# Kernel tuning notes

Hardware: AMD Instinct MI355X
Metric: run time of the kernel (lower is better)

Reference implementation:

```python
import jax, jax.numpy as jnp
import numpy as np

N = 10000      # nodes
E0 = 100000    # edges (no self loops); self loops appended -> E = E0 + N
IN = 512       # input feature dim
HID = 256      # out_channels per head
OUT = 10       # classes
H1, H2 = 4, 1  # heads conv1 / conv2
K = 5          # mixture-of-Gaussians prior components ('mixGau-5')
ON = 2 * HID   # out_neurons per head (mean | raw-std)
D1, D2 = H1 * HID, H2 * HID  # latent dims per conv
LOG2PI = float(np.log(2.0 * np.pi))


def _norm_logprob(z, mu, sigma):
    return -0.5 * jnp.square((z - mu) / sigma) - jnp.log(sigma) - 0.5 * LOG2PI


def _seg_softmax(logits, seg, n):
    # numerically stable softmax over segments defined by seg (target node ids)
    m = jax.ops.segment_max(logits, seg, num_segments=n)
    e = jnp.exp(logits - m[seg])
    s = jax.ops.segment_sum(e, seg, num_segments=n)
    return e / (s[seg] + 1e-16)


def _gib_conv(x, W, att, pi, mu, logsig, eps, gumbel, src, dst, heads):
    n = x.shape[0]
    xh = (x @ W).reshape(n, heads, ON)                       # [n,H,ON]
    # GAT attention: score(e) = leaky_relu(<x_i,att_l> + <x_j,att_r>)
    s_i = jnp.einsum('nhd,hd->nh', xh, att[:, :ON])
    s_j = jnp.einsum('nhd,hd->nh', xh, att[:, ON:])
    alpha = jax.nn.leaky_relu(s_i[dst] + s_j[src], 0.2)      # [E,H]
    alpha = _seg_softmax(alpha, dst, n)
    # structure KL vs uniform prior 1/deg
    deg = jax.ops.segment_sum(jnp.ones_like(alpha[:, 0]), dst, num_segments=n)
    prior = (1.0 / deg)[dst][:, None]
    kl = (alpha * (jnp.log(alpha + 1e-12) - jnp.log(prior + 1e-12))).sum() / alpha.size
    # categorical structural sampling: gumbel-softmax per segment
    alpha_s = _seg_softmax(jnp.log(alpha + 1e-16) + gumbel, dst, n)
    out = jax.ops.segment_sum(xh[src] * alpha_s[:, :, None], dst, num_segments=n)  # [n,H,ON]
    # per-head diag reparameterization: ON = (mean:HID | raw std:HID)
    mean = out[..., :HID].reshape(n, heads * HID)
    std = jax.nn.softplus(out[..., HID:]).reshape(n, heads * HID) + 1e-10
    Z = mean[None] + std[None] * eps                         # [S,n,D]
    log_q = _norm_logprob(Z, mean[None], std[None]).sum(-1)  # [S,n]
    # mixture-of-Gaussians feature prior, per-dimension mixture
    logpi = jax.nn.log_softmax(pi)
    comp = _norm_logprob(Z[..., None], mu, jnp.exp(logsig)) + logpi  # [S,n,D,K]
    prior_lp = jax.nn.logsumexp(comp, axis=-1).sum(-1)       # [S,n]
    ixz = (log_q - prior_lp).mean()
    return Z.mean(0), kl, ixz


def setup_inputs() -> dict:
    key = jax.random.key(0)
    ks = jax.random.split(key, 20)
    x = jax.random.normal(ks[0], (N, IN), jnp.float32)
    # edge list guaranteed free of self-loops (remove_self_loops is then a no-op)
    s = jax.random.randint(ks[1], (E0,), 0, N)
    off = jax.random.randint(ks[2], (E0,), 1, N)
    edge_index = jnp.stack([s, (s + off) % N]).astype(jnp.int32)
    E = E0 + N

    def xav(k, fi, fo):
        a = np.sqrt(6.0 / (fi + fo)).astype(np.float32)
        return jax.random.uniform(k, (fi, fo), jnp.float32, -a, a)

    def gumbel(k, shape):
        u = jax.random.uniform(k, shape, jnp.float32, 1e-6, 1.0 - 1e-6)
        return -jnp.log(-jnp.log(u))

    return {
        'x': x, 'edge_index': edge_index,
        'W1': xav(ks[3], IN, H1 * ON),
        'att1': xav(ks[4], H1, 2 * ON),
        'pi1': jnp.zeros((K,), jnp.float32),
        'mu1': jax.random.normal(ks[5], (D1, K), jnp.float32) * 0.1,
        'logsig1': jnp.zeros((D1, K), jnp.float32),
        'eps1': jax.random.normal(ks[6], (1, N, D1), jnp.float32),
        'g1': gumbel(ks[7], (E, H1)),
        'W2': xav(ks[8], D1, H2 * ON),
        'att2': xav(ks[9], H2, 2 * ON),
        'pi2': jnp.zeros((K,), jnp.float32),
        'mu2': jax.random.normal(ks[10], (D2, K), jnp.float32) * 0.1,
        'logsig2': jnp.zeros((D2, K), jnp.float32),
        'eps2': jax.random.normal(ks[11], (1, N, D2), jnp.float32),
        'g2': gumbel(ks[12], (E, H2)),
        'Wfc': xav(ks[13], D2, OUT),
        'bfc': jnp.zeros((OUT,), jnp.float32),
    }


def reference(x, edge_index, W1, att1, pi1, mu1, logsig1, eps1, g1,
              W2, att2, pi2, mu2, logsig2, eps2, g2, Wfc, bfc):
    n = x.shape[0]
    loop = jnp.arange(n, dtype=edge_index.dtype)
    src = jnp.concatenate([edge_index[0], loop])
    dst = jnp.concatenate([edge_index[1], loop])
    h, kl1, ixz1 = _gib_conv(x, W1, att1, pi1, mu1, logsig1, eps1, g1, src, dst, H1)
    h = jax.nn.elu(h)
    h, kl2, ixz2 = _gib_conv(h, W2, att2, pi2, mu2, logsig2, eps2, g2, src, dst, H2)
    h = jax.nn.elu(h)
    logits = h @ Wfc + bfc
    return logits, kl1 + kl2, ixz1 + ixz2
```

## Files before the change

kernel.cpp:

```cpp
#include <hip/hip_runtime.h>
#include <math.h>

constexpr int NN   = 10000;
constexpr int E0C  = 100000;
constexpr int EC   = E0C + NN;
constexpr int INC  = 512;
constexpr int HIDC = 256;
constexpr int OUTC = 10;
constexpr int H1C  = 4;
constexpr int H2C  = 1;
constexpr int ONC  = 2 * HIDC;
constexpr int D1C  = H1C * HIDC;
constexpr int D2C  = H2C * HIDC;
constexpr int KC   = 5;
constexpr float LOG2PI_F = 1.8378770664093453f;

using u16 = unsigned short;
typedef __attribute__((ext_vector_type(8))) short bf16x8;
typedef __attribute__((ext_vector_type(4))) float f32x4;

__device__ __forceinline__ unsigned fkey(float f) {
    unsigned b = __float_as_uint(f);
    return (b & 0x80000000u) ? ~b : (b | 0x80000000u);
}
__device__ __forceinline__ float funkey(unsigned k) {
    unsigned b = (k & 0x80000000u) ? (k & 0x7fffffffu) : ~k;
    return __uint_as_float(b);
}
__device__ __forceinline__ unsigned f2bf(float f) {
    unsigned u = __float_as_uint(f);
    return (u + 0x7fffu + ((u >> 16) & 1u)) >> 16;
}
__device__ __forceinline__ float bflo(unsigned u) { return __uint_as_float(u << 16); }
__device__ __forceinline__ float bfhi(unsigned u) { return __uint_as_float(u & 0xffff0000u); }
__device__ __forceinline__ float bf1(u16 v) { return __uint_as_float(((unsigned)v) << 16); }
__device__ __forceinline__ void edge_sd(int e, const int* __restrict__ ei, int& src, int& dst) {
    if (e < E0C) { src = ei[e]; dst = ei[E0C + e]; }
    else         { src = e - E0C; dst = src; }
}

__global__ void zero_u32(unsigned* __restrict__ p, int n) {
    int i = blockIdx.x * blockDim.x + threadIdx.x;
    if (i < n) p[i] = 0u;
}

__global__ void cast_bf16(const float* __restrict__ in, u16* __restrict__ o, int n4) {
    int i = blockIdx.x * blockDim.x + threadIdx.x;
    if (i >= n4) return;
    float4 v = ((const float4*)in)[i];
    uint2 r;
    r.x = f2bf(v.x) | (f2bf(v.y) << 16);
    r.y = f2bf(v.z) | (f2bf(v.w) << 16);
    ((uint2*)o)[i] = r;
}

__global__ __launch_bounds__(256) void transpose_cast_bf16(const float* __restrict__ W,
                                                           u16* __restrict__ WT,
                                                           int K, int N) {
    __shared__ float tile[32][33];
    int n0 = blockIdx.x * 32, k0 = blockIdx.y * 32;
    int tx = threadIdx.x, ty = threadIdx.y;
    for (int r = ty; r < 32; r += 8) tile[r][tx] = W[(size_t)(k0 + r) * N + n0 + tx];
    __syncthreads();
    for (int r = ty; r < 32; r += 8) WT[(size_t)(n0 + r) * K + k0 + tx] = (u16)f2bf(tile[tx][r]);
}

__global__ void count_deg(const int* __restrict__ ei, int* __restrict__ deg) {
    int e = blockIdx.x * blockDim.x + threadIdx.x;
    if (e >= EC) return;
    int dst = (e < E0C) ? ei[E0C + e] : (e - E0C);
    atomicAdd(&deg[dst], 1);
}

__global__ __launch_bounds__(1024) void scan_kernel(const int* __restrict__ deg,
                                                    int* __restrict__ offs,
                                                    float* __restrict__ deg_f) {
    __shared__ int part[1024];
    const int CH = (NN + 1023) / 1024;
    int tid = threadIdx.x;
    int base = tid * CH;
    int s = 0;
    for (int i = 0; i < CH; i++) { int idx = base + i; if (idx < NN) s += deg[idx]; }
    part[tid] = s;
    __syncthreads();
    for (int o = 1; o < 1024; o <<= 1) {
        int v = (tid >= o) ? part[tid - o] : 0;
        __syncthreads();
        part[tid] += v;
        __syncthreads();
    }
    int run = (tid == 0) ? 0 : part[tid - 1];
    for (int i = 0; i < CH; i++) {
        int idx = base + i;
        if (idx < NN) {
            offs[idx] = run;
            run += deg[idx];
            deg_f[idx] = (float)deg[idx];
        }
    }
    if (tid == 1023) offs[NN] = run;
}

__global__ void csr_fill(const int* __restrict__ ei, int* __restrict__ cursor,
                         const int* __restrict__ offs, int* __restrict__ csr_src,
                         int* __restrict__ pos_of_e) {
    int e = blockIdx.x * blockDim.x + threadIdx.x;
    if (e >= EC) return;
    int src, dst;
    edge_sd(e, ei, src, dst);
    int pos = offs[dst] + atomicAdd(&cursor[dst], 1);
    csr_src[pos] = src;
    pos_of_e[e] = pos;
}

template <int BM, int BN, int BK, bool BF16OUT>
__global__ __launch_bounds__(256) void mfma_gemm(const u16* __restrict__ A,
                                                 const u16* __restrict__ BT,
                                                 void* __restrict__ Cv,
                                                 int M, int N, int K) {
    constexpr int PK = BK + 16;
    __shared__ __align__(16) u16 As[BM][PK];
    __shared__ __align__(16) u16 Bs[BN][PK];
    const int tid = threadIdx.x;
    const int lane = tid & 63;
    const int wave = tid >> 6;
    const int wm = (wave & 1) * 64;
    const int wn = (wave >> 1) * 64;
    const int row0 = blockIdx.y * BM;
    const int col0 = blockIdx.x * BN;

    f32x4 acc[4][4] = {};
    const int srow = tid >> 1;
    const int shalf = (tid & 1) * 16;
    const int fr = lane & 15;
    const int fq = (lane >> 4) * 8;

    for (int k0 = 0; k0 < K; k0 += BK) {
        uint4 va0 = {0, 0, 0, 0}, va1 = {0, 0, 0, 0};
        int ga = row0 + srow;
        if (ga < M) {
            const uint4* p = (const uint4*)(A + (size_t)ga * K + k0 + shalf);
            va0 = p[0]; va1 = p[1];
        }
        const uint4* pb = (const uint4*)(BT + (size_t)(col0 + srow) * K + k0 + shalf);
        uint4 vb0 = pb[0], vb1 = pb[1];
        __syncthreads();
        *(uint4*)&As[srow][shalf]     = va0;
        *(uint4*)&As[srow][shalf + 8] = va1;
        *(uint4*)&Bs[srow][shalf]     = vb0;
        *(uint4*)&Bs[srow][shalf + 8] = vb1;
        __syncthreads();
        bf16x8 af[4], bfr[4];
#pragma unroll
        for (int i = 0; i < 4; i++) {
            af[i]  = *(const bf16x8*)&As[wm + i * 16 + fr][fq];
            bfr[i] = *(const bf16x8*)&Bs[wn + i * 16 + fr][fq];
        }
#pragma unroll
        for (int mi = 0; mi < 4; mi++)
#pragma unroll
            for (int ni = 0; ni < 4; ni++)
                acc[mi][ni] = __builtin_amdgcn_mfma_f32_16x16x32_bf16(af[mi], bfr[ni], acc[mi][ni], 0, 0, 0);
    }
    const int cc = lane & 15;
    const int cr = (lane >> 4) * 4;
#pragma unroll
    for (int mi = 0; mi < 4; mi++) {
#pragma unroll
        for (int r = 0; r < 4; r++) {
            int grow = row0 + wm + mi * 16 + cr + r;
            if (grow < M) {
#pragma unroll
                for (int ni = 0; ni < 4; ni++) {
                    int gcol = col0 + wn + ni * 16 + cc;
                    if (BF16OUT)
                        ((u16*)Cv)[(size_t)grow * N + gcol] = (u16)f2bf(acc[mi][ni][r]);
                    else
                        ((float*)Cv)[(size_t)grow * N + gcol] = acc[mi][ni][r];
                }
            }
        }
    }
}

template <int H>
__global__ __launch_bounds__(256) void scores_bf16(const u16* __restrict__ xh,
                                                   const float* __restrict__ att,
                                                   float* __restrict__ s_i,
                                                   float* __restrict__ s_j) {
    int gw = (blockIdx.x * 256 + threadIdx.x) >> 6;
    int lane = threadIdx.x & 63;
    if (gw >= NN * H) return;
    int n = gw / H, h = gw - n * H;
    const u16* xr = xh + ((size_t)n * H + h) * ONC;
    uint4 v = ((const uint4*)xr)[lane];
    float xv[8] = { bflo(v.x), bfhi(v.x), bflo(v.y), bfhi(v.y),
                    bflo(v.z), bfhi(v.z), bflo(v.w), bfhi(v.w) };
    const float* base = att + (size_t)h * 2 * ONC;
    const float4* aL = (const float4*)(base + lane * 8);
    const float4* aR = (const float4*)(base + ONC + lane * 8);
    float4 l0 = aL[0], l1 = aL[1], r0 = aR[0], r1 = aR[1];
    float ai = xv[0] * l0.x + xv[1] * l0.y + xv[2] * l0.z + xv[3] * l0.w
             + xv[4] * l1.x + xv[5] * l1.y + xv[6] * l1.z + xv[7] * l1.w;
    float aj = xv[0] * r0.x + xv[1] * r0.y + xv[2] * r0.z + xv[3] * r0.w
             + xv[4] * r1.x + xv[5] * r1.y + xv[6] * r1.z + xv[7] * r1.w;
#pragma unroll
    for (int o = 32; o > 0; o >>= 1) {
        ai += __shfl_down(ai, o, 64);
        aj += __shfl_down(aj, o, 64);
    }
    if (lane == 0) { s_i[gw] = ai; s_j[gw] = aj; }
}

template <int H>
__global__ void edge_pass1(const int* __restrict__ ei, const float* __restrict__ s_i,
                           const float* __restrict__ s_j, float* __restrict__ A,
                           unsigned* __restrict__ m1) {
    int idx = blockIdx.x * blockDim.x + threadIdx.x;
    if (idx >= EC * H) return;
    int e = idx / H, h = idx - e * H;
    int src, dst; edge_sd(e, ei, src, dst);
    float a = s_i[dst * H + h] + s_j[src * H + h];
    a = (a > 0.f) ? a : 0.2f * a;
    A[idx] = a;
    atomicMax(&m1[dst * H + h], fkey(a));
}

template <int H>
__global__ void edge_pass2(const int* __restrict__ ei, float* __restrict__ A,
                           const unsigned* __restrict__ m1, float* __restrict__ ss1) {
    int idx = blockIdx.x * blockDim.x + threadIdx.x;
    if (idx >= EC * H) return;
    int e = idx / H, h = idx - e * H;
    int src, dst; edge_sd(e, ei, src, dst);
    float ex = __expf(A[idx] - funkey(m1[dst * H + h]));
    A[idx] = ex;
    atomicAdd(&ss1[dst * H + h], ex);
}

template <int H>
__global__ __launch_bounds__(256) void edge_pass3(const int* __restrict__ ei,
                                                  const float* __restrict__ A,
                                                  const float* __restrict__ ss1,
                                                  const float* __restrict__ deg_f,
                                                  const float* __restrict__ g,
                                                  float* __restrict__ B,
                                                  unsigned* __restrict__ m2,
                                                  float* __restrict__ kl_acc,
                                                  float scale) {
    int idx = blockIdx.x * blockDim.x + threadIdx.x;
    float t = 0.f;
    if (idx < EC * H) {
        int e = idx / H, h = idx - e * H;
        int src, dst; edge_sd(e, ei, src, dst);
        float alpha = A[idx] / (ss1[dst * H + h] + 1e-16f);
        float prior = 1.0f / deg_f[dst];
        t = alpha * (__logf(alpha + 1e-12f) - __logf(prior + 1e-12f));
        float l2 = __logf(alpha + 1e-16f) + g[idx];
        B[idx] = l2;
        atomicMax(&m2[dst * H + h], fkey(l2));
    }
#pragma unroll
    for (int o = 32; o > 0; o >>= 1) t += __shfl_down(t, o, 64);
    __shared__ float red[4];
    int lane = threadIdx.x & 63, wid = threadIdx.x >> 6;
    if (lane == 0) red[wid] = t;
    __syncthreads();
    if (threadIdx.x == 0) {
        atomicAdd(kl_acc, (red[0] + red[1] + red[2] + red[3]) * scale);
    }
}

template <int H>
__global__ void edge_pass4(const int* __restrict__ ei, float* __restrict__ B,
                           const unsigned* __restrict__ m2, float* __restrict__ ss2) {
    int idx = blockIdx.x * blockDim.x + threadIdx.x;
    if (idx >= EC * H) return;
    int e = idx / H, h = idx - e * H;
    int src, dst; edge_sd(e, ei, src, dst);
    float ex = __expf(B[idx] - funkey(m2[dst * H + h]));
    B[idx] = ex;
    atomicAdd(&ss2[dst * H + h], ex);
}

template <int H>
__global__ void edge_pass5(const int* __restrict__ ei, const float* __restrict__ B,
                           const float* __restrict__ ss2, const int* __restrict__ pos_of_e,
                           float* __restrict__ Bp) {
    int idx = blockIdx.x * blockDim.x + threadIdx.x;
    if (idx >= EC * H) return;
    int e = idx / H, h = idx - e * H;
    int src, dst; edge_sd(e, ei, src, dst);
    Bp[(size_t)pos_of_e[e] * H + h] = B[idx] / (ss2[dst * H + h] + 1e-16f);
}

template <int H>
__global__ __launch_bounds__(256) void gather_bf16(const u16* __restrict__ xh,
                                                   const float* __restrict__ alpha_csr,
                                                   const int* __restrict__ offs,
                                                   const int* __restrict__ csr_src,
                                                   u16* __restrict__ out) {
    constexpr int CPE = H * ONC / 256;
    constexpr int CHK = 128;
    int n = blockIdx.x;
    int tid = threadIdx.x;
    int beg = offs[n], end = offs[n + 1];
    __shared__ int s_src[CHK];
    __shared__ __align__(16) float s_w[CHK][H];
    float acc[CPE];
#pragma unroll
    for (int j = 0; j < CPE; j++) acc[j] = 0.f;
    const int c0 = tid * CPE;
    const int head = c0 / ONC;
    for (int c = beg; c < end; c += CHK) {
        int cnt = min(CHK, end - c);
        __syncthreads();
        for (int i = tid; i < cnt; i += 256) {
            s_src[i] = csr_src[c + i];
            if (H == 4) {
                float4 w = ((const float4*)alpha_csr)[c + i];
                *(float4*)s_w[i] = w;
            } else {
                s_w[i][0] = alpha_csr[c + i];
            }
        }
        __syncthreads();
        for (int i = 0; i < cnt; i++) {
            const u16* xr = xh + (size_t)s_src[i] * (H * ONC) + c0;
            float w = s_w[i][head];
            if (CPE == 8) {
                uint4 v = *(const uint4*)xr;
                acc[0] = fmaf(w, bflo(v.x), acc[0]);
                acc[1] = fmaf(w, bfhi(v.x), acc[1]);
                acc[2] = fmaf(w, bflo(v.y), acc[2]);
                acc[3] = fmaf(w, bfhi(v.y), acc[3]);
                acc[4] = fmaf(w, bflo(v.z), acc[4]);
                acc[5] = fmaf(w, bfhi(v.z), acc[5]);
                acc[6] = fmaf(w, bflo(v.w), acc[6]);
                acc[7] = fmaf(w, bfhi(v.w), acc[7]);
            } else {
                unsigned v = *(const unsigned*)xr;
                acc[0] = fmaf(w, bflo(v), acc[0]);
                acc[1] = fmaf(w, bfhi(v), acc[1]);
            }
        }
    }
    u16* orow = out + (size_t)n * (H * ONC) + c0;
    if (CPE == 8) {
        uint4 r;
        r.x = f2bf(acc[0]) | (f2bf(acc[1]) << 16);
        r.y = f2bf(acc[2]) | (f2bf(acc[3]) << 16);
        r.z = f2bf(acc[4]) | (f2bf(acc[5]) << 16);
        r.w = f2bf(acc[6]) | (f2bf(acc[7]) << 16);
        *(uint4*)orow = r;
    } else {
        *(unsigned*)orow = f2bf(acc[0]) | (f2bf(acc[1]) << 16);
    }
}

__global__ void mix_table(const float* __restrict__ pi, const float* __restrict__ mu,
                          const float* __restrict__ logsig, float* __restrict__ tab, int DK) {
    int i = blockIdx.x * blockDim.x + threadIdx.x;
    if (i >= DK) return;
    int k = i % KC;
    float p[KC]; float mx = -3.4e38f;
#pragma unroll
    for (int j = 0; j < KC; j++) { p[j] = pi[j]; mx = fmaxf(mx, p[j]); }
    float s = 0.f;
#pragma unroll
    for (int j = 0; j < KC; j++) s += expf(p[j] - mx);
    float lpi = p[k] - (mx + logf(s));
    float ls = logsig[i];
    float inv = expf(-ls);
    float inv2 = inv * inv;
    float m = mu[i];
    tab[i]          = -0.5f * inv2;
    tab[DK + i]     = inv2 * m;
    tab[2 * DK + i] = -0.5f * inv2 * m * m - ls - 0.5f * LOG2PI_F + lpi;
}

template <int H, int NT, bool BF16OUT>
__global__ __launch_bounds__(256) void zixz3_kernel(const u16* __restrict__ in_agg,
                                                    const float* __restrict__ eps,
                                                    const float* __restrict__ tab,
                                                    void* __restrict__ hout_,
                                                    float* __restrict__ ixz_acc) {
    constexpr int D = H * HIDC;
    constexpr int DK = D * KC;
    const int tid = threadIdx.x;
    const int h = blockIdx.y;
    const int d = h * HIDC + tid;
    float ca[KC], cb[KC], cc[KC];
#pragma unroll
    for (int k = 0; k < KC; k++) {
        ca[k] = tab[d * KC + k];
        cb[k] = tab[DK + d * KC + k];
        cc[k] = tab[2 * DK + d * KC + k];
    }
    const int n0 = blockIdx.x * NT;
    float local = 0.f;
#pragma unroll 1
    for (int nn = 0; nn < NT; nn++) {
        int n = n0 + nn;
        const u16* orow = in_agg + ((size_t)n * H + h) * ONC;
        float mean = bf1(orow[tid]);
        float raw  = bf1(orow[HIDC + tid]);
        float sp = fmaxf(raw, 0.f) + __logf(1.f + __expf(-fabsf(raw)));
        float stdv = sp + 1e-10f;
        float ep = eps[(size_t)n * D + d];
        float Z = fmaf(stdv, ep, mean);
        float hv = (Z > 0.f) ? Z : (__expf(Z) - 1.f);
        if (BF16OUT) ((u16*)hout_)[(size_t)n * D + d] = (u16)f2bf(hv);
        else         ((float*)hout_)[(size_t)n * D + d] = hv;
        float logq = fmaf(-0.5f, ep * ep, -__logf(stdv)) - 0.5f * LOG2PI_F;
        float comp[KC]; float mx = -3.4e38f;
#pragma unroll
        for (int k = 0; k < KC; k++) {
            float cv = fmaf(fmaf(ca[k], Z, cb[k]), Z, cc[k]);
            comp[k] = cv;
            mx = fmaxf(mx, cv);
        }
        float se = 0.f;
#pragma unroll
        for (int k = 0; k < KC; k++) se += __expf(comp[k] - mx);
        local += logq - (mx + __logf(se));
    }
#pragma unroll
    for (int o = 32; o > 0; o >>= 1) local += __shfl_down(local, o, 64);
    __shared__ float red[4];
    int lane = tid & 63, wid = tid >> 6;
    if (lane == 0) red[wid] = local;
    __syncthreads();
    if (tid == 0) {
        atomicAdd(ixz_acc, (red[0] + red[1] + red[2] + red[3]) * (1.0f / NN));
    }
}

__global__ void fc_kernel(const float* __restrict__ h, const float* __restrict__ W,
                          const float* __restrict__ b, float* __restrict__ out) {
    int idx = blockIdx.x * blockDim.x + threadIdx.x;
    if (idx >= NN * OUTC) return;
    int n = idx / OUTC, o = idx - n * OUTC;
    const float* hr = h + (size_t)n * D2C;
    float acc = b[o];
#pragma unroll 8
    for (int c = 0; c < D2C; c++) acc += hr[c] * W[c * OUTC + o];
    out[idx] = acc;
}

extern "C" void kernel_launch(void* const* d_in, const int* in_sizes, int n_in,
                              void* d_out, int out_size, void* d_ws, size_t ws_size,
                              hipStream_t stream) {
    (void)in_sizes; (void)n_in; (void)out_size; (void)ws_size;
    const float* x       = (const float*)d_in[0];
    const int*   ei      = (const int*)d_in[1];
    const float* W1      = (const float*)d_in[2];
    const float* att1    = (const float*)d_in[3];
    const float* pi1     = (const float*)d_in[4];
    const float* mu1     = (const float*)d_in[5];
    const float* logsig1 = (const float*)d_in[6];
    const float* eps1    = (const float*)d_in[7];
    const float* g1      = (const float*)d_in[8];
    const float* W2      = (const float*)d_in[9];
    const float* att2    = (const float*)d_in[10];
    const float* pi2     = (const float*)d_in[11];
    const float* mu2     = (const float*)d_in[12];
    const float* logsig2 = (const float*)d_in[13];
    const float* eps2    = (const float*)d_in[14];
    const float* g2      = (const float*)d_in[15];
    const float* Wfc     = (const float*)d_in[16];
    const float* bfc     = (const float*)d_in[17];
    float* out = (float*)d_out;

    char* ws = (char*)d_ws;
    const size_t szAB = (size_t)NN * 2048 * sizeof(float);
    char* regA = ws;
    char* regB = ws + szAB;
    size_t cur = 2 * szAB;
    auto alloc = [&](size_t bytes) -> char* {
        char* p = ws + cur;
        cur += (bytes + 255) & ~(size_t)255;
        return p;
    };
    float*    alphaA  = (float*)alloc((size_t)EC * H1C * sizeof(float));
    float*    alphaB  = (float*)alloc((size_t)EC * H1C * sizeof(float));
    float*    s_i     = (float*)alloc((size_t)NN * H1C * sizeof(float));
    float*    s_j     = (float*)alloc((size_t)NN * H1C * sizeof(float));
    unsigned* stats   = (unsigned*)alloc((size_t)4 * NN * H1C * sizeof(unsigned));
    unsigned* m1  = stats;
    float*    ss1 = (float*)(stats + (size_t)NN * H1C);
    unsigned* m2  = stats + (size_t)2 * NN * H1C;
    float*    ss2 = (float*)(stats + (size_t)3 * NN * H1C);
    int*   deg_i    = (int*)alloc(NN * sizeof(int));
    float* deg_f    = (float*)alloc(NN * sizeof(float));
    int*   offs     = (int*)alloc((NN + 1) * sizeof(int));
    int*   cursor   = (int*)alloc(NN * sizeof(int));
    int*   csr_src  = (int*)alloc(EC * sizeof(int));
    int*   pos_of_e = (int*)alloc(EC * sizeof(int));
    u16*   xb1     = (u16*)alloc((size_t)NN * INC * sizeof(u16));
    u16*   w1t     = (u16*)alloc((size_t)2048 * 512 * sizeof(u16));
    u16*   w2t     = (u16*)alloc((size_t)512 * 1024 * sizeof(u16));
    float* tab1    = (float*)alloc((size_t)3 * D1C * KC * sizeof(float));
    float* tab2    = (float*)alloc((size_t)3 * D2C * KC * sizeof(float));

    u16*   xh1b = (u16*)regA;
    u16*   out1 = (u16*)regB;
    u16*   h1b  = (u16*)regA;
    u16*   xh2b = (u16*)regB;
    u16*   out2 = (u16*)regA;
    float* h2   = (float*)(regB + (size_t)NN * 512 * sizeof(u16));
    float* kl_acc  = out + (size_t)NN * OUTC;
    float* ixz_acc = kl_acc + 1;

    const int ZB = 256;
    zero_u32<<<(NN + ZB - 1) / ZB, ZB, 0, stream>>>((unsigned*)deg_i, NN);
    zero_u32<<<(NN + ZB - 1) / ZB, ZB, 0, stream>>>((unsigned*)cursor, NN);
    zero_u32<<<(4 * NN * H1C + ZB - 1) / ZB, ZB, 0, stream>>>(stats, 4 * NN * H1C);
    zero_u32<<<1, ZB, 0, stream>>>((unsigned*)kl_acc, 2);

    count_deg<<<(EC + ZB - 1) / ZB, ZB, 0, stream>>>(ei, deg_i);
    scan_kernel<<<1, 1024, 0, stream>>>(deg_i, offs, deg_f);
    csr_fill<<<(EC + ZB - 1) / ZB, ZB, 0, stream>>>(ei, cursor, offs, csr_src, pos_of_e);

    cast_bf16<<<(NN * INC / 4 + ZB - 1) / ZB, ZB, 0, stream>>>(x, xb1, NN * INC / 4);
    transpose_cast_bf16<<<dim3(2048 / 32, 512 / 32), dim3(32, 8), 0, stream>>>(W1, w1t, 512, 2048);
    transpose_cast_bf16<<<dim3(512 / 32, 1024 / 32), dim3(32, 8), 0, stream>>>(W2, w2t, 1024, 512);
    mix_table<<<(D1C * KC + ZB - 1) / ZB, ZB, 0, stream>>>(pi1, mu1, logsig1, tab1, D1C * KC);
    mix_table<<<(D2C * KC + ZB - 1) / ZB, ZB, 0, stream>>>(pi2, mu2, logsig2, tab2, D2C * KC);

    const int EB1 = (EC * H1C + ZB - 1) / ZB;
    const int EB2 = (EC * H2C + ZB - 1) / ZB;
    const int MG = (NN + 127) / 128;

    mfma_gemm<128, 128, 32, true><<<dim3(2048 / 128, MG), 256, 0, stream>>>(xb1, w1t, xh1b, NN, 2048, 512);
    scores_bf16<H1C><<<(NN * H1C + 3) / 4, 256, 0, stream>>>(xh1b, att1, s_i, s_j);
    edge_pass1<H1C><<<EB1, ZB, 0, stream>>>(ei, s_i, s_j, alphaA, m1);
    edge_pass2<H1C><<<EB1, ZB, 0, stream>>>(ei, alphaA, m1, ss1);
    edge_pass3<H1C><<<EB1, ZB, 0, stream>>>(ei, alphaA, ss1, deg_f, g1, alphaA, m2, kl_acc,
                                            1.0f / (float)(EC * H1C));
    edge_pass4<H1C><<<EB1, ZB, 0, stream>>>(ei, alphaA, m2, ss2);
    edge_pass5<H1C><<<EB1, ZB, 0, stream>>>(ei, alphaA, ss2, pos_of_e, alphaB);
    gather_bf16<H1C><<<NN, 256, 0, stream>>>(xh1b, alphaB, offs, csr_src, out1);
    zixz3_kernel<H1C, 25, true><<<dim3(NN / 25, H1C), 256, 0, stream>>>(out1, eps1, tab1, (void*)h1b, ixz_acc);

    zero_u32<<<(4 * NN * H1C + ZB - 1) / ZB, ZB, 0, stream>>>(stats, 4 * NN * H1C);
    mfma_gemm<128, 128, 32, true><<<dim3(512 / 128, MG), 256, 0, stream>>>(h1b, w2t, xh2b, NN, 512, 1024);
    scores_bf16<H2C><<<(NN * H2C + 3) / 4, 256, 0, stream>>>(xh2b, att2, s_i, s_j);
    edge_pass1<H2C><<<EB2, ZB, 0, stream>>>(ei, s_i, s_j, alphaA, m1);
    edge_pass2<H2C><<<EB2, ZB, 0, stream>>>(ei, alphaA, m1, ss1);
    edge_pass3<H2C><<<EB2, ZB, 0, stream>>>(ei, alphaA, ss1, deg_f, g2, alphaA, m2, kl_acc,
                                            1.0f / (float)(EC * H2C));
    edge_pass4<H2C><<<EB2, ZB, 0, stream>>>(ei, alphaA, m2, ss2);
    edge_pass5<H2C><<<EB2, ZB, 0, stream>>>(ei, alphaA, ss2, pos_of_e, alphaB);
    gather_bf16<H2C><<<NN, 256, 0, stream>>>(xh2b, alphaB, offs, csr_src, out2);
    zixz3_kernel<H2C, 10, false><<<dim3(NN / 10, H2C), 256, 0, stream>>>(out2, eps2, tab2, (void*)h2, ixz_acc);

    fc_kernel<<<(NN * OUTC + ZB - 1) / ZB, ZB, 0, stream>>>(h2, Wfc, bfc, out);
}
```

Baseline: 521.5 us.

## Fuse edge softmax passes into per-node CSR wave kernel and panelize gather

Replaces the five per-edge attention passes, which used global atomicMax/atomicAdd on per-node stats, with a single kernel that walks each target node's CSR segment in one wave. It computes both segment softmaxes and the KL term with wave reductions and writes alpha directly in CSR order. The KL is rewritten algebraically using log-sum-exp, which drops the epsilon terms. The gather is also split into column panels with one wave per node, giving more parallel blocks and smaller per-thread loads. This removes atomics, stat zeroing and intermediate edge arrays, but the gumbel reads become indirect, lanes sit idle on low-degree nodes, and each panel block re-reads the same CSR indices.

```diff
diff --git a/kernel.cpp b/kernel.cpp
--- a/kernel.cpp
+++ b/kernel.cpp
@@ -19,14 +19,6 @@
 typedef __attribute__((ext_vector_type(8))) short bf16x8;
 typedef __attribute__((ext_vector_type(4))) float f32x4;
 
-__device__ __forceinline__ unsigned fkey(float f) {
-    unsigned b = __float_as_uint(f);
-    return (b & 0x80000000u) ? ~b : (b | 0x80000000u);
-}
-__device__ __forceinline__ float funkey(unsigned k) {
-    unsigned b = (k & 0x80000000u) ? (k & 0x7fffffffu) : ~k;
-    return __uint_as_float(b);
-}
 __device__ __forceinline__ unsigned f2bf(float f) {
     unsigned u = __float_as_uint(f);
     return (u + 0x7fffu + ((u >> 16) & 1u)) >> 16;
@@ -37,6 +29,16 @@
 __device__ __forceinline__ void edge_sd(int e, const int* __restrict__ ei, int& src, int& dst) {
     if (e < E0C) { src = ei[e]; dst = ei[E0C + e]; }
     else         { src = e - E0C; dst = src; }
+}
+__device__ __forceinline__ float wmax(float x) {
+#pragma unroll
+    for (int o = 32; o > 0; o >>= 1) x = fmaxf(x, __shfl_xor(x, o, 64));
+    return x;
+}
+__device__ __forceinline__ float wsum(float x) {
+#pragma unroll
+    for (int o = 32; o > 0; o >>= 1) x += __shfl_xor(x, o, 64);
+    return x;
 }
 
 __global__ void zero_u32(unsigned* __restrict__ p, int n) {
@@ -73,8 +75,7 @@
 }
 
 __global__ __launch_bounds__(1024) void scan_kernel(const int* __restrict__ deg,
-                                                    int* __restrict__ offs,
-                                                    float* __restrict__ deg_f) {
+                                                    int* __restrict__ offs) {
     __shared__ int part[1024];
     const int CH = (NN + 1023) / 1024;
     int tid = threadIdx.x;
@@ -95,7 +96,6 @@
         if (idx < NN) {
             offs[idx] = run;
             run += deg[idx];
-            deg_f[idx] = (float)deg[idx];
         }
     }
     if (tid == 1023) offs[NN] = run;
@@ -103,14 +103,14 @@
 
 __global__ void csr_fill(const int* __restrict__ ei, int* __restrict__ cursor,
                          const int* __restrict__ offs, int* __restrict__ csr_src,
-                         int* __restrict__ pos_of_e) {
+                         int* __restrict__ csr_eid) {
     int e = blockIdx.x * blockDim.x + threadIdx.x;
     if (e >= EC) return;
     int src, dst;
     edge_sd(e, ei, src, dst);
     int pos = offs[dst] + atomicAdd(&cursor[dst], 1);
     csr_src[pos] = src;
-    pos_of_e[e] = pos;
+    csr_eid[pos] = e;
 }
 
 template <int BM, int BN, int BK, bool BF16OUT>
@@ -212,147 +212,137 @@
     if (lane == 0) { s_i[gw] = ai; s_j[gw] = aj; }
 }
 
-template <int H>
-__global__ void edge_pass1(const int* __restrict__ ei, const float* __restrict__ s_i,
-                           const float* __restrict__ s_j, float* __restrict__ A,
-                           unsigned* __restrict__ m1) {
-    int idx = blockIdx.x * blockDim.x + threadIdx.x;
-    if (idx >= EC * H) return;
-    int e = idx / H, h = idx - e * H;
-    int src, dst; edge_sd(e, ei, src, dst);
-    float a = s_i[dst * H + h] + s_j[src * H + h];
-    a = (a > 0.f) ? a : 0.2f * a;
-    A[idx] = a;
-    atomicMax(&m1[dst * H + h], fkey(a));
-}
-
-template <int H>
-__global__ void edge_pass2(const int* __restrict__ ei, float* __restrict__ A,
-                           const unsigned* __restrict__ m1, float* __restrict__ ss1) {
-    int idx = blockIdx.x * blockDim.x + threadIdx.x;
-    if (idx >= EC * H) return;
-    int e = idx / H, h = idx - e * H;
-    int src, dst; edge_sd(e, ei, src, dst);
-    float ex = __expf(A[idx] - funkey(m1[dst * H + h]));
-    A[idx] = ex;
-    atomicAdd(&ss1[dst * H + h], ex);
-}
-
-template <int H>
-__global__ __launch_bounds__(256) void edge_pass3(const int* __restrict__ ei,
-                                                  const float* __restrict__ A,
-                                                  const float* __restrict__ ss1,
-                                                  const float* __restrict__ deg_f,
+template <int H, int PW>
+__global__ __launch_bounds__(256) void attn_fused(const int* __restrict__ offs,
+                                                  const int* __restrict__ csr_src,
+                                                  const int* __restrict__ csr_eid,
+                                                  const float* __restrict__ s_i,
+                                                  const float* __restrict__ s_j,
                                                   const float* __restrict__ g,
-                                                  float* __restrict__ B,
-                                                  unsigned* __restrict__ m2,
+                                                  float* __restrict__ alpha_csr,
                                                   float* __restrict__ kl_acc,
                                                   float scale) {
-    int idx = blockIdx.x * blockDim.x + threadIdx.x;
-    float t = 0.f;
-    if (idx < EC * H) {
-        int e = idx / H, h = idx - e * H;
-        int src, dst; edge_sd(e, ei, src, dst);
-        float alpha = A[idx] / (ss1[dst * H + h] + 1e-16f);
-        float prior = 1.0f / deg_f[dst];
-        t = alpha * (__logf(alpha + 1e-12f) - __logf(prior + 1e-12f));
-        float l2 = __logf(alpha + 1e-16f) + g[idx];
-        B[idx] = l2;
-        atomicMax(&m2[dst * H + h], fkey(l2));
-    }
-#pragma unroll
-    for (int o = 32; o > 0; o >>= 1) t += __shfl_down(t, o, 64);
+    const int tid = threadIdx.x;
+    const int wave = tid >> 6, lane = tid & 63;
+    const int pair0 = (blockIdx.x * 4 + wave) * PW;
+    float kl = 0.f;
+#pragma unroll 1
+    for (int t = 0; t < PW; t++) {
+        int pr = pair0 + t;
+        if (pr >= NN * H) break;
+        int n = pr / H, h = pr - (pr / H) * H;
+        int beg = offs[n], end = offs[n + 1];
+        int deg = end - beg;
+        float si = s_i[n * H + h];
+        float ldeg = __logf((float)deg);
+        if (deg <= 64) {
+            int pos = beg + lane;
+            bool v = lane < deg;
+            int src = v ? csr_src[pos] : 0;
+            int eid = v ? csr_eid[pos] : 0;
+            float a = si + s_j[src * H + h];
+            a = (a > 0.f) ? a : 0.2f * a;
+            if (!v) a = -3.4e38f;
+            float m1 = wmax(a);
+            float am = v ? (a - m1) : 0.f;
+            float e1 = v ? __expf(am) : 0.f;
+            float ss1 = wsum(e1);
+            float sd  = wsum(e1 * am);
+            float lss1 = __logf(ss1);
+            kl += sd / ss1 - lss1 + ldeg;
+            float l2 = v ? (am - lss1 + g[eid * H + h]) : -3.4e38f;
+            float m2 = wmax(l2);
+            float e2 = v ? __expf(l2 - m2) : 0.f;
+            float ss2 = wsum(e2);
+            if (v) alpha_csr[(size_t)pos * H + h] = e2 / ss2;
+        } else {
+            float m1 = -3.4e38f;
+            for (int p = beg + lane; p < end; p += 64) {
+                float a = si + s_j[csr_src[p] * H + h];
+                a = (a > 0.f) ? a : 0.2f * a;
+                m1 = fmaxf(m1, a);
+            }
+            m1 = wmax(m1);
+            float ss1 = 0.f, sd = 0.f;
+            for (int p = beg + lane; p < end; p += 64) {
+                float a = si + s_j[csr_src[p] * H + h];
+                a = (a > 0.f) ? a : 0.2f * a;
+                float e1 = __expf(a - m1);
+                ss1 += e1; sd += e1 * (a - m1);
+            }
+            ss1 = wsum(ss1); sd = wsum(sd);
+            float lss1 = __logf(ss1);
+            kl += sd / ss1 - lss1 + ldeg;
+            float m2 = -3.4e38f;
+            for (int p = beg + lane; p < end; p += 64) {
+                float a = si + s_j[csr_src[p] * H + h];
+                a = (a > 0.f) ? a : 0.2f * a;
+                m2 = fmaxf(m2, a - m1 - lss1 + g[csr_eid[p] * H + h]);
+            }
+            m2 = wmax(m2);
+            float ss2 = 0.f;
+            for (int p = beg + lane; p < end; p += 64) {
+                float a = si + s_j[csr_src[p] * H + h];
+                a = (a > 0.f) ? a : 0.2f * a;
+                ss2 += __expf(a - m1 - lss1 + g[csr_eid[p] * H + h] - m2);
+            }
+            ss2 = wsum(ss2);
+            for (int p = beg + lane; p < end; p += 64) {
+                float a = si + s_j[csr_src[p] * H + h];
+                a = (a > 0.f) ? a : 0.2f * a;
+                alpha_csr[(size_t)p * H + h] =
+                    __expf(a - m1 - lss1 + g[csr_eid[p] * H + h] - m2) / ss2;
+            }
+        }
+    }
     __shared__ float red[4];
-    int lane = threadIdx.x & 63, wid = threadIdx.x >> 6;
-    if (lane == 0) red[wid] = t;
+    if (lane == 0) red[wave] = kl;
     __syncthreads();
-    if (threadIdx.x == 0) {
+    if (tid == 0)
         atomicAdd(kl_acc, (red[0] + red[1] + red[2] + red[3]) * scale);
-    }
-}
-
-template <int H>
-__global__ void edge_pass4(const int* __restrict__ ei, float* __restrict__ B,
-                           const unsigned* __restrict__ m2, float* __restrict__ ss2) {
-    int idx = blockIdx.x * blockDim.x + threadIdx.x;
-    if (idx >= EC * H) return;
-    int e = idx / H, h = idx - e * H;
-    int src, dst; edge_sd(e, ei, src, dst);
-    float ex = __expf(B[idx] - funkey(m2[dst * H + h]));
-    B[idx] = ex;
-    atomicAdd(&ss2[dst * H + h], ex);
-}
-
-template <int H>
-__global__ void edge_pass5(const int* __restrict__ ei, const float* __restrict__ B,
-                           const float* __restrict__ ss2, const int* __restrict__ pos_of_e,
-                           float* __restrict__ Bp) {
-    int idx = blockIdx.x * blockDim.x + threadIdx.x;
-    if (idx >= EC * H) return;
-    int e = idx / H, h = idx - e * H;
-    int src, dst; edge_sd(e, ei, src, dst);
-    Bp[(size_t)pos_of_e[e] * H + h] = B[idx] / (ss2[dst * H + h] + 1e-16f);
-}
-
-template <int H>
-__global__ __launch_bounds__(256) void gather_bf16(const u16* __restrict__ xh,
-                                                   const float* __restrict__ alpha_csr,
-                                                   const int* __restrict__ offs,
-                                                   const int* __restrict__ csr_src,
-                                                   u16* __restrict__ out) {
-    constexpr int CPE = H * ONC / 256;
-    constexpr int CHK = 128;
-    int n = blockIdx.x;
-    int tid = threadIdx.x;
-    int beg = offs[n], end = offs[n + 1];
-    __shared__ int s_src[CHK];
-    __shared__ __align__(16) float s_w[CHK][H];
-    float acc[CPE];
-#pragma unroll
-    for (int j = 0; j < CPE; j++) acc[j] = 0.f;
-    const int c0 = tid * CPE;
-    const int head = c0 / ONC;
-    for (int c = beg; c < end; c += CHK) {
-        int cnt = min(CHK, end - c);
-        __syncthreads();
-        for (int i = tid; i < cnt; i += 256) {
-            s_src[i] = csr_src[c + i];
-            if (H == 4) {
-                float4 w = ((const float4*)alpha_csr)[c + i];
-                *(float4*)s_w[i] = w;
-            } else {
-                s_w[i][0] = alpha_csr[c + i];
-            }
-        }
-        __syncthreads();
-        for (int i = 0; i < cnt; i++) {
-            const u16* xr = xh + (size_t)s_src[i] * (H * ONC) + c0;
-            float w = s_w[i][head];
-            if (CPE == 8) {
-                uint4 v = *(const uint4*)xr;
-                acc[0] = fmaf(w, bflo(v.x), acc[0]);
-                acc[1] = fmaf(w, bfhi(v.x), acc[1]);
-                acc[2] = fmaf(w, bflo(v.y), acc[2]);
-                acc[3] = fmaf(w, bfhi(v.y), acc[3]);
-                acc[4] = fmaf(w, bflo(v.z), acc[4]);
-                acc[5] = fmaf(w, bfhi(v.z), acc[5]);
-                acc[6] = fmaf(w, bflo(v.w), acc[6]);
-                acc[7] = fmaf(w, bfhi(v.w), acc[7]);
-            } else {
-                unsigned v = *(const unsigned*)xr;
-                acc[0] = fmaf(w, bflo(v), acc[0]);
-                acc[1] = fmaf(w, bfhi(v), acc[1]);
-            }
-        }
-    }
-    u16* orow = out + (size_t)n * (H * ONC) + c0;
-    if (CPE == 8) {
-        uint4 r;
+}
+
+template <int H, int NP>
+__global__ __launch_bounds__(256) void gather_panel(const u16* __restrict__ xh,
+                                                    const float* __restrict__ alpha_csr,
+                                                    const int* __restrict__ offs,
+                                                    const int* __restrict__ csr_src,
+                                                    u16* __restrict__ out) {
+    constexpr int ROW = H * ONC;
+    constexpr int CPP = ROW / NP;
+    constexpr int CL  = CPP / 64;
+    const int bx = blockIdx.x;
+    const int panel = bx % NP;
+    const int n = (bx / NP) * 4 + (threadIdx.x >> 6);
+    const int lane = threadIdx.x & 63;
+    const int head = (panel * CPP) / ONC;
+    const int c0 = panel * CPP + lane * CL;
+    const int beg = offs[n], end = offs[n + 1];
+    float acc[CL];
+#pragma unroll
+    for (int j = 0; j < CL; j++) acc[j] = 0.f;
+    for (int p = beg; p < end; ++p) {
+        int src = csr_src[p];
+        float w = alpha_csr[(size_t)p * H + head];
+        const u16* xr = xh + (size_t)src * ROW + c0;
+        if (CL == 4) {
+            uint2 v = *(const uint2*)xr;
+            acc[0] = fmaf(w, bflo(v.x), acc[0]);
+            acc[1] = fmaf(w, bfhi(v.x), acc[1]);
+            acc[2] = fmaf(w, bflo(v.y), acc[2]);
+            acc[3] = fmaf(w, bfhi(v.y), acc[3]);
+        } else {
+            unsigned v = *(const unsigned*)xr;
+            acc[0] = fmaf(w, bflo(v), acc[0]);
+            acc[1] = fmaf(w, bfhi(v), acc[1]);
+        }
+    }
+    u16* orow = out + (size_t)n * ROW + c0;
+    if (CL == 4) {
+        uint2 r;
         r.x = f2bf(acc[0]) | (f2bf(acc[1]) << 16);
         r.y = f2bf(acc[2]) | (f2bf(acc[3]) << 16);
-        r.z = f2bf(acc[4]) | (f2bf(acc[5]) << 16);
-        r.w = f2bf(acc[6]) | (f2bf(acc[7]) << 16);
-        *(uint4*)orow = r;
+        *(uint2*)orow = r;
     } else {
         *(unsigned*)orow = f2bf(acc[0]) | (f2bf(acc[1]) << 16);
     }
@@ -482,21 +472,14 @@
         cur += (bytes + 255) & ~(size_t)255;
         return p;
     };
-    float*    alphaA  = (float*)alloc((size_t)EC * H1C * sizeof(float));
-    float*    alphaB  = (float*)alloc((size_t)EC * H1C * sizeof(float));
-    float*    s_i     = (float*)alloc((size_t)NN * H1C * sizeof(float));
-    float*    s_j     = (float*)alloc((size_t)NN * H1C * sizeof(float));
-    unsigned* stats   = (unsigned*)alloc((size_t)4 * NN * H1C * sizeof(unsigned));
-    unsigned* m1  = stats;
-    float*    ss1 = (float*)(stats + (size_t)NN * H1C);
-    unsigned* m2  = stats + (size_t)2 * NN * H1C;
-    float*    ss2 = (float*)(stats + (size_t)3 * NN * H1C);
+    float* alphaB   = (float*)alloc((size_t)EC * H1C * sizeof(float));
+    float* s_i      = (float*)alloc((size_t)NN * H1C * sizeof(float));
+    float* s_j      = (float*)alloc((size_t)NN * H1C * sizeof(float));
     int*   deg_i    = (int*)alloc(NN * sizeof(int));
-    float* deg_f    = (float*)alloc(NN * sizeof(float));
     int*   offs     = (int*)alloc((NN + 1) * sizeof(int));
     int*   cursor   = (int*)alloc(NN * sizeof(int));
     int*   csr_src  = (int*)alloc(EC * sizeof(int));
-    int*   pos_of_e = (int*)alloc(EC * sizeof(int));
+    int*   csr_eid  = (int*)alloc(EC * sizeof(int));
     u16*   xb1     = (u16*)alloc((size_t)NN * INC * sizeof(u16));
     u16*   w1t     = (u16*)alloc((size_t)2048 * 512 * sizeof(u16));
     u16*   w2t     = (u16*)alloc((size_t)512 * 1024 * sizeof(u16));
@@ -515,12 +498,11 @@
     const int ZB = 256;
     zero_u32<<<(NN + ZB - 1) / ZB, ZB, 0, stream>>>((unsigned*)deg_i, NN);
     zero_u32<<<(NN + ZB - 1) / ZB, ZB, 0, stream>>>((unsigned*)cursor, NN);
-    zero_u32<<<(4 * NN * H1C + ZB - 1) / ZB, ZB, 0, stream>>>(stats, 4 * NN * H1C);
     zero_u32<<<1, ZB, 0, stream>>>((unsigned*)kl_acc, 2);
 
     count_deg<<<(EC + ZB - 1) / ZB, ZB, 0, stream>>>(ei, deg_i);
-    scan_kernel<<<1, 1024, 0, stream>>>(deg_i, offs, deg_f);
-    csr_fill<<<(EC + ZB - 1) / ZB, ZB, 0, stream>>>(ei, cursor, offs, csr_src, pos_of_e);
+    scan_kernel<<<1, 1024, 0, stream>>>(deg_i, offs);
+    csr_fill<<<(EC + ZB - 1) / ZB, ZB, 0, stream>>>(ei, cursor, offs, csr_src, csr_eid);
 
     cast_bf16<<<(NN * INC / 4 + ZB - 1) / ZB, ZB, 0, stream>>>(x, xb1, NN * INC / 4);
     transpose_cast_bf16<<<dim3(2048 / 32, 512 / 32), dim3(32, 8), 0, stream>>>(W1, w1t, 512, 2048);
@@ -528,31 +510,22 @@
     mix_table<<<(D1C * KC + ZB - 1) / ZB, ZB, 0, stream>>>(pi1, mu1, logsig1, tab1, D1C * KC);
     mix_table<<<(D2C * KC + ZB - 1) / ZB, ZB, 0, stream>>>(pi2, mu2, logsig2, tab2, D2C * KC);
 
-    const int EB1 = (EC * H1C + ZB - 1) / ZB;
-    const int EB2 = (EC * H2C + ZB - 1) / ZB;
     const int MG = (NN + 127) / 128;
 
     mfma_gemm<128, 128, 32, true><<<dim3(2048 / 128, MG), 256, 0, stream>>>(xb1, w1t, xh1b, NN, 2048, 512);
     scores_bf16<H1C><<<(NN * H1C + 3) / 4, 256, 0, stream>>>(xh1b, att1, s_i, s_j);
-    edge_pass1<H1C><<<EB1, ZB, 0, stream>>>(ei, s_i, s_j, alphaA, m1);
-    edge_pass2<H1C><<<EB1, ZB, 0, stream>>>(ei, alphaA, m1, ss1);
-    edge_pass3<H1C><<<EB1, ZB, 0, stream>>>(ei, alphaA, ss1, deg_f, g1, alphaA, m2, kl_acc,
-                                            1.0f / (float)(EC * H1C));
-    edge_pass4<H1C><<<EB1, ZB, 0, stream>>>(ei, alphaA, m2, ss2);
-    edge_pass5<H1C><<<EB1, ZB, 0, stream>>>(ei, alphaA, ss2, pos_of_e, alphaB);
-    gather_bf16<H1C><<<NN, 256, 0, stream>>>(xh1b, alphaB, offs, csr_src, out1);
+    attn_fused<H1C, 8><<<(NN * H1C + 31) / 32, 256, 0, stream>>>(offs, csr_src, csr_eid,
+                                                                 s_i, s_j, g1, alphaB, kl_acc,
+                                                                 1.0f / (float)(EC * H1C));
+    gather_panel<H1C, 8><<<8 * (NN / 4), 256, 0, stream>>>(xh1b, alphaB, offs, csr_src, out1);
     zixz3_kernel<H1C, 25, true><<<dim3(NN / 25, H1C), 256, 0, stream>>>(out1, eps1, tab1, (void*)h1b, ixz_acc);
 
-    zero_u32<<<(4 * NN * H1C + ZB - 1) / ZB, ZB, 0, stream>>>(stats, 4 * NN * H1C);
     mfma_gemm<128, 128, 32, true><<<dim3(512 / 128, MG), 256, 0, stream>>>(h1b, w2t, xh2b, NN, 512, 1024);
     scores_bf16<H2C><<<(NN * H2C + 3) / 4, 256, 0, stream>>>(xh2b, att2, s_i, s_j);
-    edge_pass1<H2C><<<EB2, ZB, 0, stream>>>(ei, s_i, s_j, alphaA, m1);
-    edge_pass2<H2C><<<EB2, ZB, 0, stream>>>(ei, alphaA, m1, ss1);
-    edge_pass3<H2C><<<EB2, ZB, 0, stream>>>(ei, alphaA, ss1, deg_f, g2, alphaA, m2, kl_acc,
-                                            1.0f / (float)(EC * H2C));
-    edge_pass4<H2C><<<EB2, ZB, 0, stream>>>(ei, alphaA, m2, ss2);
-    edge_pass5<H2C><<<EB2, ZB, 0, stream>>>(ei, alphaA, ss2, pos_of_e, alphaB);
-    gather_bf16<H2C><<<NN, 256, 0, stream>>>(xh2b, alphaB, offs, csr_src, out2);
+    attn_fused<H2C, 8><<<(NN * H2C + 31) / 32, 256, 0, stream>>>(offs, csr_src, csr_eid,
+                                                                 s_i, s_j, g2, alphaB, kl_acc,
+                                                                 1.0f / (float)(EC * H2C));
+    gather_panel<H2C, 4><<<4 * (NN / 4), 256, 0, stream>>>(xh2b, alphaB, offs, csr_src, out2);
     zixz3_kernel<H2C, 10, false><<<dim3(NN / 10, H2C), 256, 0, stream>>>(out2, eps2, tab2, (void*)h2, ixz_acc);
 
     fc_kernel<<<(NN * OUTC + ZB - 1) / ZB, ZB, 0, stream>>>(h2, Wfc, bfc, out);
```

After: 508.1 us. 2.6% less time.
